# Performance work log

Measured on AMD Instinct MI355X. Metric: run time of the kernel, lower is better.

The kernel has to match this reference:

```python
import jax, jax.numpy as jnp
import numpy as np

ASSIGN_TEMP = 0.1
BATCH_SIZE = 16
NUM_PROTOTYPES = 1024
EMBD_DIM = 512


def setup_inputs() -> dict:
    key = jax.random.key(0)
    k1, k2 = jax.random.split(key)
    feature_maps = jax.random.normal(k1, (BATCH_SIZE, EMBD_DIM, 64, 64), dtype=jnp.float32)
    prototypes = jax.random.normal(k2, (1, NUM_PROTOTYPES, EMBD_DIM), dtype=jnp.float32)
    return {"feature_maps": feature_maps, "prototypes": prototypes}


def reference(feature_maps, prototypes):
    # assign_nearest_clusters
    bs, c, h, w = feature_maps.shape
    K = prototypes.shape[1]
    # [N, c] pixel embeddings (channels-last flatten, as movedim(1,3).reshape)
    x = feature_maps.transpose(0, 2, 3, 1).reshape(-1, c)
    p = prototypes[0]  # [K, c]
    d2 = (jnp.sum(x * x, axis=1, keepdims=True)
          + jnp.sum(p * p, axis=1)[None, :]
          - 2.0 * (x @ p.T))
    dist = jnp.sqrt(jnp.maximum(d2, 0.0))  # [N, K]
    sims = jax.nn.softmax(-dist / ASSIGN_TEMP, axis=1)  # [N, K]
    sims = sims.reshape(bs, h, w, K).transpose(0, 3, 1, 2)  # [bs, K, h, w]
    nearest = jnp.argmax(sims, axis=1)  # [bs, h, w]
    onehot = jax.nn.one_hot(nearest, K, dtype=jnp.int32)  # [bs, h, w, K]
    counts = onehot.sum(axis=(1, 2))  # [bs, K] pixels per prototype
    mask = (counts > 3).sum()
    return sims, mask.astype(jnp.float32) / BATCH_SIZE
```

## Files before the change

kernel.cpp:

```cpp
#include <hip/hip_runtime.h>
#include <hip/hip_bf16.h>

typedef _Float16 f16x8 __attribute__((ext_vector_type(8)));
typedef float    f32x4 __attribute__((ext_vector_type(4)));

#define NPROTO 1024
#define EMB    512
#define NB     16
#define HW     4096
#define NPIX   (NB * HW)
#define INV_TEMP 10.0f

__global__ void prep_protos(const float* __restrict__ proto,
                            _Float16* __restrict__ Ph,
                            float* __restrict__ pnorm) {
    int k = blockIdx.x;
    int t = threadIdx.x;
    const float* src = proto + (size_t)k * EMB + t * 8;
    float4 v0 = ((const float4*)src)[0];
    float4 v1 = ((const float4*)src)[1];
    float sq = v0.x*v0.x + v0.y*v0.y + v0.z*v0.z + v0.w*v0.w
             + v1.x*v1.x + v1.y*v1.y + v1.z*v1.z + v1.w*v1.w;
    f16x8 h;
    h[0] = (_Float16)v0.x; h[1] = (_Float16)v0.y; h[2] = (_Float16)v0.z; h[3] = (_Float16)v0.w;
    h[4] = (_Float16)v1.x; h[5] = (_Float16)v1.y; h[6] = (_Float16)v1.z; h[7] = (_Float16)v1.w;
    *(f16x8*)(Ph + (size_t)k * EMB + t * 8) = h;
#pragma unroll
    for (int m = 1; m < 64; m <<= 1) sq += __shfl_xor(sq, m);
    if (t == 0) pnorm[k] = sq;
}

__global__ void zero_counts(int* __restrict__ counts) {
    int i = blockIdx.x * blockDim.x + threadIdx.x;
    if (i < NB * NPROTO) counts[i] = 0;
}

__global__ __launch_bounds__(512, 1)
void assign_main(const float* __restrict__ fm, const _Float16* __restrict__ Ph,
                 const float* __restrict__ pnorm, int* __restrict__ counts,
                 float* __restrict__ out) {
    __shared__ __align__(16) unsigned char Ald[NPROTO * 64];
    __shared__ __align__(16) unsigned char Bld[32 * 64];
    __shared__ float pn_lds[NPROTO];
    __shared__ float xnsum[16 * 32];
    __shared__ float xn[32];
    __shared__ float redmax[256];
    __shared__ float redsum[256];
    __shared__ float argv_[256];
    __shared__ int   argk_[256];

    const int t    = threadIdx.x;
    const int lane = t & 63, wid = t >> 6;
    const int lrow = lane >> 4;
    const int lcol = lane & 15;

    const int n0  = blockIdx.x * 32;
    const int b   = n0 >> 12;
    const int hw0 = n0 & 4095;

    pn_lds[t]       = pnorm[t];
    pn_lds[t + 512] = pnorm[t + 512];

    f32x4 acc[8][2];
#pragma unroll
    for (int i = 0; i < 8; ++i)
#pragma unroll
        for (int j = 0; j < 2; ++j)
#pragma unroll
            for (int e = 0; e < 4; ++e) acc[i][j][e] = 0.0f;

    float sq = 0.0f;
    const int bpx = t & 31;
    const int bcg = t >> 5;
    const float* fmB = fm + (size_t)b * EMB * HW + hw0;

    for (int ks = 0; ks < 16; ++ks) {
        const int c0 = ks * 32;
#pragma unroll
        for (int p = 0; p < 8; ++p) {
            int k  = p * 128 + (t >> 2);
            int cg = t & 3;
            uint4 v = *(const uint4*)(Ph + (size_t)k * EMB + c0 + cg * 8);
            int off = k * 64 + ((cg * 16) ^ ((k & 3) << 4));
            *(uint4*)(Ald + off) = v;
        }
#pragma unroll
        for (int p = 0; p < 2; ++p) {
            int c = bcg + p * 16;
            float v = fmB[(size_t)(c0 + c) * HW + bpx];
            sq += v * v;
            int off = bpx * 64 + ((c * 2) ^ ((bpx & 3) << 4));
            *(_Float16*)(Bld + off) = (_Float16)v;
        }
        __syncthreads();

        f16x8 bf[2];
#pragma unroll
        for (int nf = 0; nf < 2; ++nf) {
            int px  = nf * 16 + lcol;
            int off = px * 64 + ((lrow * 16) ^ ((px & 3) << 4));
            bf[nf] = *(const f16x8*)(Bld + off);
        }
#pragma unroll
        for (int mf = 0; mf < 8; ++mf) {
            int r   = wid * 128 + mf * 16 + lcol;
            int off = r * 64 + ((lrow * 16) ^ ((r & 3) << 4));
            f16x8 af = *(const f16x8*)(Ald + off);
            acc[mf][0] = __builtin_amdgcn_mfma_f32_16x16x32_f16(af, bf[0], acc[mf][0], 0, 0, 0);
            acc[mf][1] = __builtin_amdgcn_mfma_f32_16x16x32_f16(af, bf[1], acc[mf][1], 0, 0, 0);
        }
        __syncthreads();
    }

    xnsum[bcg * 32 + bpx] = sq;
    __syncthreads();
    if (t < 32) {
        float s = 0.0f;
#pragma unroll
        for (int g = 0; g < 16; ++g) s += xnsum[g * 32 + t];
        xn[t] = s;
    }
    __syncthreads();

    float lmax[2] = {-1e30f, -1e30f};
    float lav[2]  = {-1e30f, -1e30f};
    int   lak[2]  = {0, 0};
#pragma unroll
    for (int mf = 0; mf < 8; ++mf) {
#pragma unroll
        for (int nf = 0; nf < 2; ++nf) {
            int px = nf * 16 + lcol;
#pragma unroll
            for (int j = 0; j < 4; ++j) {
                int kidx = wid * 128 + mf * 16 + lrow * 4 + j;
                float d2 = xn[px] + pn_lds[kidx] - 2.0f * acc[mf][nf][j];
                float lg = -INV_TEMP * sqrtf(fmaxf(d2, 0.0f));
                acc[mf][nf][j] = lg;
                if (lg > lav[nf]) { lav[nf] = lg; lak[nf] = kidx; }
                lmax[nf] = fmaxf(lmax[nf], lg);
            }
        }
    }
#pragma unroll
    for (int nf = 0; nf < 2; ++nf) {
#pragma unroll
        for (int m = 16; m <= 32; m <<= 1) {
            float ov = __shfl_xor(lav[nf], m);
            int   ok = __shfl_xor(lak[nf], m);
            if (ov > lav[nf] || (ov == lav[nf] && ok < lak[nf])) { lav[nf] = ov; lak[nf] = ok; }
            lmax[nf] = fmaxf(lmax[nf], __shfl_xor(lmax[nf], m));
        }
    }
    if (lane < 16) {
#pragma unroll
        for (int nf = 0; nf < 2; ++nf) {
            int idx = wid * 32 + nf * 16 + lane;
            redmax[idx] = lmax[nf];
            argv_[idx]  = lav[nf];
            argk_[idx]  = lak[nf];
        }
    }
    __syncthreads();

    float gmax[2];
#pragma unroll
    for (int nf = 0; nf < 2; ++nf) {
        int col = nf * 16 + lcol;
        float gm = -1e30f, gav = -1e30f;
        int gak = 0;
#pragma unroll
        for (int w = 0; w < 8; ++w) {
            gm = fmaxf(gm, redmax[w * 32 + col]);
            float av = argv_[w * 32 + col];
            int   ak = argk_[w * 32 + col];
            if (av > gav || (av == gav && ak < gak)) { gav = av; gak = ak; }
        }
        gmax[nf] = gm;
        if (wid == 0 && lrow == 0) atomicAdd(&counts[b * NPROTO + gak], 1);

        float s = 0.0f;
#pragma unroll
        for (int mf = 0; mf < 8; ++mf)
#pragma unroll
            for (int j = 0; j < 4; ++j) {
                float e = expf(acc[mf][nf][j] - gm);
                acc[mf][nf][j] = e;
                s += e;
            }
        s += __shfl_xor(s, 16);
        s += __shfl_xor(s, 32);
        if (lane < 16) redsum[wid * 32 + nf * 16 + lane] = s;
    }
    __syncthreads();

    const size_t obase = (size_t)b * NPROTO * HW + hw0;
#pragma unroll
    for (int nf = 0; nf < 2; ++nf) {
        int col = nf * 16 + lcol;
        float s = 0.0f;
#pragma unroll
        for (int w = 0; w < 8; ++w) s += redsum[w * 32 + col];
        float inv = 1.0f / s;
#pragma unroll
        for (int mf = 0; mf < 8; ++mf)
#pragma unroll
            for (int j = 0; j < 4; ++j) {
                int kidx = wid * 128 + mf * 16 + lrow * 4 + j;
                out[obase + (size_t)kidx * HW + col] = acc[mf][nf][j] * inv;
            }
    }
}

__global__ void finalize(const int* __restrict__ counts, float* __restrict__ out) {
    int t = threadIdx.x;
    int local = 0;
    for (int i = t; i < NB * NPROTO; i += 256) local += (counts[i] > 3) ? 1 : 0;
#pragma unroll
    for (int m = 1; m < 64; m <<= 1) local += __shfl_xor(local, m);
    __shared__ int wsum[4];
    if ((t & 63) == 0) wsum[t >> 6] = local;
    __syncthreads();
    if (t == 0) out[(size_t)NPIX * NPROTO] = (float)(wsum[0] + wsum[1] + wsum[2] + wsum[3]) / 16.0f;
}

extern "C" void kernel_launch(void* const* d_in, const int* in_sizes, int n_in,
                              void* d_out, int out_size, void* d_ws, size_t ws_size,
                              hipStream_t stream) {
    const float* fm    = (const float*)d_in[0];
    const float* proto = (const float*)d_in[1];
    float* out = (float*)d_out;

    char* ws = (char*)d_ws;
    _Float16* Ph   = (_Float16*)ws;
    float*    pnorm = (float*)(ws + (size_t)NPROTO * EMB * 2);
    int*      counts = (int*)(ws + (size_t)NPROTO * EMB * 2 + 4096);

    prep_protos<<<NPROTO, 64, 0, stream>>>(proto, Ph, pnorm);
    zero_counts<<<(NB * NPROTO + 255) / 256, 256, 0, stream>>>(counts);
    assign_main<<<NPIX / 32, 512, 0, stream>>>(fm, Ph, pnorm, counts, out);
    finalize<<<1, 256, 0, stream>>>(counts, out);
}
```

Baseline: 266.1 us.

## Double-buffer prototype tiles via direct global-to-LDS loads with 64-pixel blocks

The main kernel now handles 64 pixels per block with 1024 threads, so each prototype tile staged in LDS is reused across twice as many pixels. Prototype slices move straight from global memory into LDS through global_load_lds, and the A and B tiles are double-buffered so the next K-slice loads while the current one feeds the MFMAs. The per-step sync count drops from two to one. The change also swaps expf for __expf and reuses LDS for the reduction scratch. In exchange it needs about 140KB of LDS per block and more waves per block, which caps occupancy at one block per CU.

```diff
diff --git a/kernel.cpp b/kernel.cpp
--- a/kernel.cpp
+++ b/kernel.cpp
@@ -1,7 +1,9 @@
 #include <hip/hip_runtime.h>
 #include <hip/hip_bf16.h>
+#include <stdint.h>
 
 typedef _Float16 f16x8 __attribute__((ext_vector_type(8)));
+typedef _Float16 f16x2 __attribute__((ext_vector_type(2)));
 typedef float    f32x4 __attribute__((ext_vector_type(4)));
 
 #define NPROTO 1024
@@ -10,6 +12,8 @@
 #define HW     4096
 #define NPIX   (NB * HW)
 #define INV_TEMP 10.0f
+#define TPX    64
+#define NTHR   1024
 
 __global__ void prep_protos(const float* __restrict__ proto,
                             _Float16* __restrict__ Ph,
@@ -35,105 +39,128 @@
     if (i < NB * NPROTO) counts[i] = 0;
 }
 
-__global__ __launch_bounds__(512, 1)
+__global__ __launch_bounds__(NTHR)
 void assign_main(const float* __restrict__ fm, const _Float16* __restrict__ Ph,
                  const float* __restrict__ pnorm, int* __restrict__ counts,
                  float* __restrict__ out) {
-    __shared__ __align__(16) unsigned char Ald[NPROTO * 64];
-    __shared__ __align__(16) unsigned char Bld[32 * 64];
-    __shared__ float pn_lds[NPROTO];
-    __shared__ float xnsum[16 * 32];
-    __shared__ float xn[32];
-    __shared__ float redmax[256];
-    __shared__ float redsum[256];
-    __shared__ float argv_[256];
-    __shared__ int   argk_[256];
+    __shared__ __align__(16) unsigned char smem[143360];
+    unsigned char* Abuf = smem;
+    unsigned char* Bbuf = smem + 131072;
+    float* pn           = (float*)(smem + 139264);
+    float* redmax = (float*)(smem);
+    float* redsum = (float*)(smem + 4096);
+    float* argv_  = (float*)(smem + 8192);
+    int*   argk_  = (int*)  (smem + 12288);
+    float* xnsum  = (float*)(smem + 16384);
+    float* xn     = (float*)(smem + 20480);
 
     const int t    = threadIdx.x;
     const int lane = t & 63, wid = t >> 6;
     const int lrow = lane >> 4;
     const int lcol = lane & 15;
 
-    const int n0  = blockIdx.x * 32;
+    const int n0  = blockIdx.x * TPX;
     const int b   = n0 >> 12;
     const int hw0 = n0 & 4095;
 
-    pn_lds[t]       = pnorm[t];
-    pn_lds[t + 512] = pnorm[t + 512];
-
-    f32x4 acc[8][2];
-#pragma unroll
-    for (int i = 0; i < 8; ++i)
-#pragma unroll
-        for (int j = 0; j < 2; ++j)
+    pn[t] = pnorm[t];
+
+    f32x4 acc[4][4];
+#pragma unroll
+    for (int i = 0; i < 4; ++i)
+#pragma unroll
+        for (int j = 0; j < 4; ++j)
 #pragma unroll
             for (int e = 0; e < 4; ++e) acc[i][j][e] = 0.0f;
 
+    const int bpx = t & 63;
+    const int bc  = (t >> 6) << 1;
+    const float* fmB = fm + (size_t)b * EMB * HW + hw0 + bpx;
     float sq = 0.0f;
-    const int bpx = t & 31;
-    const int bcg = t >> 5;
-    const float* fmB = fm + (size_t)b * EMB * HW + hw0;
-
+    float bv0, bv1;
+
+    auto stageA = [&](int cur, int ks) {
+        const int c0 = ks * 32;
+#pragma unroll
+        for (int p = 0; p < 4; ++p) {
+            int k  = p * 256 + wid * 16 + (lane >> 2);
+            int cg = (lane & 3) ^ (k & 3);
+            const _Float16* src = Ph + (size_t)k * EMB + c0 + cg * 8;
+            __builtin_amdgcn_global_load_lds(
+                (const __attribute__((address_space(1))) void*)src,
+                (__attribute__((address_space(3))) void*)(Abuf + cur * 65536 + p * 16384 + wid * 1024),
+                16, 0, 0);
+        }
+    };
+    auto loadB = [&](int ks) {
+        const float* p0 = fmB + (size_t)(ks * 32 + bc) * HW;
+        bv0 = p0[0];
+        bv1 = p0[HW];
+    };
+    auto writeB = [&](int cur) {
+        sq += bv0 * bv0 + bv1 * bv1;
+        f16x2 h; h[0] = (_Float16)bv0; h[1] = (_Float16)bv1;
+        int slot = (bc >> 3) ^ (bpx & 3);
+        *(f16x2*)(Bbuf + cur * 4096 + bpx * 64 + (slot << 4) + (bc & 7) * 2) = h;
+    };
+
+    stageA(0, 0);
+    loadB(0);
+    writeB(0);
+    __syncthreads();
+
+    int cur = 0;
     for (int ks = 0; ks < 16; ++ks) {
-        const int c0 = ks * 32;
-#pragma unroll
-        for (int p = 0; p < 8; ++p) {
-            int k  = p * 128 + (t >> 2);
-            int cg = t & 3;
-            uint4 v = *(const uint4*)(Ph + (size_t)k * EMB + c0 + cg * 8);
-            int off = k * 64 + ((cg * 16) ^ ((k & 3) << 4));
-            *(uint4*)(Ald + off) = v;
-        }
-#pragma unroll
-        for (int p = 0; p < 2; ++p) {
-            int c = bcg + p * 16;
-            float v = fmB[(size_t)(c0 + c) * HW + bpx];
-            sq += v * v;
-            int off = bpx * 64 + ((c * 2) ^ ((bpx & 3) << 4));
-            *(_Float16*)(Bld + off) = (_Float16)v;
-        }
+        if (ks < 15) {
+            stageA(cur ^ 1, ks + 1);
+            loadB(ks + 1);
+        }
+        f16x8 bf[4];
+#pragma unroll
+        for (int nf = 0; nf < 4; ++nf) {
+            int px   = nf * 16 + lcol;
+            int slot = lrow ^ (px & 3);
+            bf[nf] = *(const f16x8*)(Bbuf + cur * 4096 + px * 64 + (slot << 4));
+        }
+#pragma unroll
+        for (int mf = 0; mf < 4; ++mf) {
+            int r    = wid * 64 + mf * 16 + lcol;
+            int slot = lrow ^ (r & 3);
+            f16x8 af = *(const f16x8*)(Abuf + cur * 65536 + r * 64 + (slot << 4));
+#pragma unroll
+            for (int nf = 0; nf < 4; ++nf)
+                acc[mf][nf] = __builtin_amdgcn_mfma_f32_16x16x32_f16(af, bf[nf], acc[mf][nf], 0, 0, 0);
+        }
+        if (ks < 15) writeB(cur ^ 1);
         __syncthreads();
-
-        f16x8 bf[2];
-#pragma unroll
-        for (int nf = 0; nf < 2; ++nf) {
-            int px  = nf * 16 + lcol;
-            int off = px * 64 + ((lrow * 16) ^ ((px & 3) << 4));
-            bf[nf] = *(const f16x8*)(Bld + off);
-        }
-#pragma unroll
-        for (int mf = 0; mf < 8; ++mf) {
-            int r   = wid * 128 + mf * 16 + lcol;
-            int off = r * 64 + ((lrow * 16) ^ ((r & 3) << 4));
-            f16x8 af = *(const f16x8*)(Ald + off);
-            acc[mf][0] = __builtin_amdgcn_mfma_f32_16x16x32_f16(af, bf[0], acc[mf][0], 0, 0, 0);
-            acc[mf][1] = __builtin_amdgcn_mfma_f32_16x16x32_f16(af, bf[1], acc[mf][1], 0, 0, 0);
-        }
-        __syncthreads();
-    }
-
-    xnsum[bcg * 32 + bpx] = sq;
-    __syncthreads();
-    if (t < 32) {
+        cur ^= 1;
+    }
+
+    xnsum[(t >> 6) * 64 + bpx] = sq;
+    __syncthreads();
+    if (t < 64) {
         float s = 0.0f;
 #pragma unroll
-        for (int g = 0; g < 16; ++g) s += xnsum[g * 32 + t];
+        for (int g = 0; g < 16; ++g) s += xnsum[g * 64 + t];
         xn[t] = s;
     }
     __syncthreads();
 
-    float lmax[2] = {-1e30f, -1e30f};
-    float lav[2]  = {-1e30f, -1e30f};
-    int   lak[2]  = {0, 0};
-#pragma unroll
-    for (int mf = 0; mf < 8; ++mf) {
-#pragma unroll
-        for (int nf = 0; nf < 2; ++nf) {
-            int px = nf * 16 + lcol;
+    float xnv[4];
+#pragma unroll
+    for (int nf = 0; nf < 4; ++nf) xnv[nf] = xn[nf * 16 + lcol];
+
+    float lmax[4] = {-1e30f, -1e30f, -1e30f, -1e30f};
+    float lav[4]  = {-1e30f, -1e30f, -1e30f, -1e30f};
+    int   lak[4]  = {0, 0, 0, 0};
+#pragma unroll
+    for (int mf = 0; mf < 4; ++mf) {
+#pragma unroll
+        for (int nf = 0; nf < 4; ++nf) {
 #pragma unroll
             for (int j = 0; j < 4; ++j) {
-                int kidx = wid * 128 + mf * 16 + lrow * 4 + j;
-                float d2 = xn[px] + pn_lds[kidx] - 2.0f * acc[mf][nf][j];
+                int kidx = wid * 64 + mf * 16 + lrow * 4 + j;
+                float d2 = xnv[nf] + pn[kidx] - 2.0f * acc[mf][nf][j];
                 float lg = -INV_TEMP * sqrtf(fmaxf(d2, 0.0f));
                 acc[mf][nf][j] = lg;
                 if (lg > lav[nf]) { lav[nf] = lg; lak[nf] = kidx; }
@@ -142,7 +169,7 @@
         }
     }
 #pragma unroll
-    for (int nf = 0; nf < 2; ++nf) {
+    for (int nf = 0; nf < 4; ++nf) {
 #pragma unroll
         for (int m = 16; m <= 32; m <<= 1) {
             float ov = __shfl_xor(lav[nf], m);
@@ -153,8 +180,8 @@
     }
     if (lane < 16) {
 #pragma unroll
-        for (int nf = 0; nf < 2; ++nf) {
-            int idx = wid * 32 + nf * 16 + lane;
+        for (int nf = 0; nf < 4; ++nf) {
+            int idx = wid * 64 + nf * 16 + lane;
             redmax[idx] = lmax[nf];
             argv_[idx]  = lav[nf];
             argk_[idx]  = lak[nf];
@@ -162,51 +189,51 @@
     }
     __syncthreads();
 
-    float gmax[2];
-#pragma unroll
-    for (int nf = 0; nf < 2; ++nf) {
-        int col = nf * 16 + lcol;
+    float gmax[4];
+#pragma unroll
+    for (int nf = 0; nf < 4; ++nf) {
+        int px = nf * 16 + lcol;
         float gm = -1e30f, gav = -1e30f;
         int gak = 0;
 #pragma unroll
-        for (int w = 0; w < 8; ++w) {
-            gm = fmaxf(gm, redmax[w * 32 + col]);
-            float av = argv_[w * 32 + col];
-            int   ak = argk_[w * 32 + col];
+        for (int w = 0; w < 16; ++w) {
+            gm = fmaxf(gm, redmax[w * 64 + px]);
+            float av = argv_[w * 64 + px];
+            int   ak = argk_[w * 64 + px];
             if (av > gav || (av == gav && ak < gak)) { gav = av; gak = ak; }
         }
         gmax[nf] = gm;
-        if (wid == 0 && lrow == 0) atomicAdd(&counts[b * NPROTO + gak], 1);
+        if (wid == 0 && lane < 16) atomicAdd(&counts[b * NPROTO + gak], 1);
 
         float s = 0.0f;
 #pragma unroll
-        for (int mf = 0; mf < 8; ++mf)
+        for (int mf = 0; mf < 4; ++mf)
 #pragma unroll
             for (int j = 0; j < 4; ++j) {
-                float e = expf(acc[mf][nf][j] - gm);
+                float e = __expf(acc[mf][nf][j] - gm);
                 acc[mf][nf][j] = e;
                 s += e;
             }
         s += __shfl_xor(s, 16);
         s += __shfl_xor(s, 32);
-        if (lane < 16) redsum[wid * 32 + nf * 16 + lane] = s;
+        if (lane < 16) redsum[wid * 64 + nf * 16 + lane] = s;
     }
     __syncthreads();
 
     const size_t obase = (size_t)b * NPROTO * HW + hw0;
 #pragma unroll
-    for (int nf = 0; nf < 2; ++nf) {
-        int col = nf * 16 + lcol;
+    for (int nf = 0; nf < 4; ++nf) {
+        int px = nf * 16 + lcol;
         float s = 0.0f;
 #pragma unroll
-        for (int w = 0; w < 8; ++w) s += redsum[w * 32 + col];
+        for (int w = 0; w < 16; ++w) s += redsum[w * 64 + px];
         float inv = 1.0f / s;
 #pragma unroll
-        for (int mf = 0; mf < 8; ++mf)
+        for (int mf = 0; mf < 4; ++mf)
 #pragma unroll
             for (int j = 0; j < 4; ++j) {
-                int kidx = wid * 128 + mf * 16 + lrow * 4 + j;
-                out[obase + (size_t)kidx * HW + col] = acc[mf][nf][j] * inv;
+                int kidx = wid * 64 + mf * 16 + lrow * 4 + j;
+                out[obase + (size_t)kidx * HW + px] = acc[mf][nf][j] * inv;
             }
     }
 }
@@ -231,12 +258,12 @@
     float* out = (float*)d_out;
 
     char* ws = (char*)d_ws;
-    _Float16* Ph   = (_Float16*)ws;
-    float*    pnorm = (float*)(ws + (size_t)NPROTO * EMB * 2);
+    _Float16* Ph     = (_Float16*)ws;
+    float*    pnorm  = (float*)(ws + (size_t)NPROTO * EMB * 2);
     int*      counts = (int*)(ws + (size_t)NPROTO * EMB * 2 + 4096);
 
     prep_protos<<<NPROTO, 64, 0, stream>>>(proto, Ph, pnorm);
     zero_counts<<<(NB * NPROTO + 255) / 256, 256, 0, stream>>>(counts);
-    assign_main<<<NPIX / 32, 512, 0, stream>>>(fm, Ph, pnorm, counts, out);
+    assign_main<<<NPIX / TPX, NTHR, 0, stream>>>(fm, Ph, pnorm, counts, out);
     finalize<<<1, 256, 0, stream>>>(counts, out);
 }
```

After: 299.5 us. +12.5%, slower.
